# Kernel tuning notes

Measured on AMD Instinct MI355X. Metric: run time of the kernel, lower is better.

Reference implementation:

```python
import jax, jax.numpy as jnp
import numpy as np

C_IN = 128
DIM = 2 * C_IN          # ELAN final channels = 2*in_channels = 256
WS = 8                  # window size
HEADS = 8
HEAD_DIM = DIM // HEADS
B, H, W = 4, 128, 128
LN_EPS = 1e-5


def setup_inputs() -> dict:
    key = jax.random.key(0)
    ks = jax.random.split(key, 20)
    mid = C_IN // 2  # middle_channels == block_channels == 64

    def p(k, shape, scale=0.05):
        return jax.random.normal(k, shape, jnp.float32) * scale

    return dict(
        x=jax.random.normal(ks[0], (B, C_IN, H, W), jnp.float32),
        # ELAN stem 1x1 convs: [main, short], each folded BN (scale, bias)
        w_stem=p(ks[1], (2, mid, C_IN, 1, 1)),
        s_stem=1.0 + p(ks[2], (2, mid)),
        b_stem=p(ks[3], (2, mid)),
        # 2 blocks x 2 convs of 3x3, mid->mid
        w_blk=p(ks[4], (4, mid, mid, 3, 3)),
        s_blk=1.0 + p(ks[5], (4, mid)),
        b_blk=p(ks[6], (4, mid)),
        # SwinV2 block params
        norm1_g=jnp.ones((DIM,), jnp.float32),
        norm1_b=jnp.zeros((DIM,), jnp.float32),
        qkv_w=p(ks[7], (3 * DIM, DIM)),
        qkv_b=p(ks[8], (3 * DIM,)).at[DIM:2 * DIM].set(0.0),  # V2 zeroes k bias
        proj_w=p(ks[9], (DIM, DIM)),
        proj_b=p(ks[10], (DIM,)),
        logit_scale=jnp.full((HEADS, 1, 1), float(np.log(10.0)), jnp.float32),
        cpb_w1=p(ks[11], (512, 2)),
        cpb_b1=p(ks[12], (512,)),
        cpb_w2=p(ks[13], (HEADS, 512)),
        norm2_g=jnp.ones((DIM,), jnp.float32),
        norm2_b=jnp.zeros((DIM,), jnp.float32),
        mlp_w1=p(ks[14], (DIM, DIM)),  # mlp_ratio=1.0
        mlp_b1=p(ks[15], (DIM,)),
        mlp_w2=p(ks[16], (DIM, DIM)),
        mlp_b2=p(ks[17], (DIM,)),
    )


def convbn(x, w, s, b, pad):
    # Conv(no bias) + eval-mode BN folded into per-channel scale/bias + SiLU
    y = jax.lax.conv_general_dilated(
        x, w, (1, 1), [(pad, pad), (pad, pad)],
        dimension_numbers=("NCHW", "OIHW", "NCHW"))
    y = y * s[None, :, None, None] + b[None, :, None, None]
    return jax.nn.silu(y)


def layernorm(x, g, b):
    m = jnp.mean(x, -1, keepdims=True)
    v = jnp.var(x, -1, keepdims=True)
    return (x - m) * jax.lax.rsqrt(v + LN_EPS) * g + b


def _rel_bias_consts():
    ws = WS
    ch = np.arange(-(ws - 1), ws, dtype=np.float32)
    table = np.stack(np.meshgrid(ch, ch, indexing="ij"), axis=-1)  # [2ws-1,2ws-1,2]
    table = table / (ws - 1) * 8.0
    table = np.sign(table) * np.log2(np.abs(table) + 1.0) / 3.0
    coords = np.stack(np.meshgrid(np.arange(ws), np.arange(ws), indexing="ij")).reshape(2, -1)
    rel = (coords[:, :, None] - coords[:, None, :]).transpose(1, 2, 0)  # [N,N,2]
    rel[..., 0] += ws - 1
    rel[..., 1] += ws - 1
    rel[..., 0] *= 2 * ws - 1
    idx = rel.sum(-1).reshape(-1)
    return jnp.asarray(table.reshape(-1, 2)), jnp.asarray(idx)


_TABLE, _IDX = _rel_bias_consts()


def elan_swin(x, w_stem, s_stem, b_stem, w_blk, s_blk, b_blk, norm1_g, norm1_b,
              qkv_w, qkv_b, proj_w, proj_b, logit_scale, cpb_w1, cpb_b1, cpb_w2,
              norm2_g, norm2_b, mlp_w1, mlp_b1, mlp_w2, mlp_b2):
    # ---- ELANBlock ----
    x_short = convbn(x, w_stem[1], s_stem[1], b_stem[1], 0)
    x_main = convbn(x, w_stem[0], s_stem[0], b_stem[0], 0)
    xb = x_main
    outs = []
    for i in range(2):
        xb = convbn(xb, w_blk[2 * i], s_blk[2 * i], b_blk[2 * i], 1)
        xb = convbn(xb, w_blk[2 * i + 1], s_blk[2 * i + 1], b_blk[2 * i + 1], 1)
        outs.append(xb)
    e = jnp.concatenate([outs[1], outs[0], x_main, x_short], axis=1)  # [B,DIM,H,W]
    e = e.transpose(0, 2, 3, 1)  # NHWC

    # ---- ShiftedWindowAttentionV2 (shift=0, H,W divisible by WS) ----
    Bn, Hh, Ww, Cc = e.shape
    nH, nW = Hh // WS, Ww // WS
    N = WS * WS
    xw = e.reshape(Bn, nH, WS, nW, WS, Cc).transpose(0, 1, 3, 2, 4, 5).reshape(-1, N, Cc)
    qkv = xw @ qkv_w.T + qkv_b
    qkv = qkv.reshape(-1, N, 3, HEADS, HEAD_DIM).transpose(2, 0, 3, 1, 4)
    q, k, v = qkv[0], qkv[1], qkv[2]  # [Bw, heads, N, d]
    qn = q / jnp.maximum(jnp.linalg.norm(q, axis=-1, keepdims=True), 1e-12)
    kn = k / jnp.maximum(jnp.linalg.norm(k, axis=-1, keepdims=True), 1e-12)
    attn = jnp.einsum("whnd,whmd->whnm", qn, kn)
    scale = jnp.exp(jnp.minimum(logit_scale, jnp.log(100.0)))  # [heads,1,1]
    attn = attn * scale[None]
    # continuous position bias MLP
    bias = jax.nn.relu(_TABLE @ cpb_w1.T + cpb_b1) @ cpb_w2.T  # [(2ws-1)^2, heads]
    bias = bias[_IDX].reshape(N, N, HEADS).transpose(2, 0, 1)
    bias = 16.0 * jax.nn.sigmoid(bias)
    attn = jax.nn.softmax(attn + bias[None], axis=-1)
    out = jnp.einsum("whnm,whmd->whnd", attn, v).transpose(0, 2, 1, 3).reshape(-1, N, Cc)
    out = out @ proj_w.T + proj_b
    out = out.reshape(Bn, nH, nW, WS, WS, Cc).transpose(0, 1, 3, 2, 4, 5).reshape(Bn, Hh, Ww, Cc)

    # ---- SwinTransformerBlockV2 (post-norm residuals) ----
    s = e + layernorm(out, norm1_g, norm1_b)
    h = s @ mlp_w1.T + mlp_b1
    h = jax.nn.gelu(h, approximate=False)
    h = h @ mlp_w2.T + mlp_b2
    s = s + layernorm(h, norm2_g, norm2_b)
    return s.transpose(0, 3, 1, 2)  # NCHW


def reference(x, w_stem, s_stem, b_stem, w_blk, s_blk, b_blk, norm1_g, norm1_b,
              qkv_w, qkv_b, proj_w, proj_b, logit_scale, cpb_w1, cpb_b1, cpb_w2,
              norm2_g, norm2_b, mlp_w1, mlp_b1, mlp_w2, mlp_b2):
    return elan_swin(x, w_stem, s_stem, b_stem, w_blk, s_blk, b_blk, norm1_g, norm1_b,
                     qkv_w, qkv_b, proj_w, proj_b, logit_scale, cpb_w1, cpb_b1, cpb_w2,
                     norm2_g, norm2_b, mlp_w1, mlp_b1, mlp_w2, mlp_b2)
```

## Files before the change

kernel.cpp:

```cpp
#include <hip/hip_runtime.h>
#include <hip/hip_bf16.h>
#include <math.h>


#define HW 16384
typedef unsigned int u32;
typedef unsigned short u16;
typedef __attribute__((ext_vector_type(8))) short short8;
typedef __attribute__((ext_vector_type(4))) float floatx4;

#define MEMBAR() asm volatile("" ::: "memory")

__device__ __forceinline__ float silu_f(float y) { return y / (1.f + expf(-y)); }
__device__ __forceinline__ float bflo(u32 u) { return __uint_as_float(u << 16); }
__device__ __forceinline__ float bfhi(u32 u) { return __uint_as_float(u & 0xffff0000u); }
__device__ __forceinline__ float bf2f(u16 v) { return __uint_as_float((u32)v << 16); }
__device__ __forceinline__ u16 f2bf(float x) {
  u32 u = __float_as_uint(x);
  u += 0x7fffu + ((u >> 16) & 1u);
  return (u16)(u >> 16);
}
__device__ __forceinline__ u32 pack2(float a, float b) {
  return (u32)f2bf(a) | ((u32)f2bf(b) << 16);
}

#define GLDS16(gp, lp)                                           \
  __builtin_amdgcn_global_load_lds(                              \
      (const __attribute__((address_space(1))) void*)(gp),       \
      (__attribute__((address_space(3))) void*)(lp), 16, 0, 0)

__global__ __launch_bounds__(256) void repack_kernel(
    const float* __restrict__ w_blk, const float* __restrict__ s_blk,
    const float* __restrict__ w_stem, const float* __restrict__ s_stem,
    u16* __restrict__ wtc, u16* __restrict__ wts) {
  int idx = blockIdx.x * 256 + threadIdx.x;
  if (idx < 147456) {
    int c = idx & 63;
    int rest = idx >> 6;
    int oc = rest & 63;
    int ct = rest >> 6;
    int conv = ct / 9, t = ct % 9;
    float w = w_blk[((size_t)(conv * 64 + oc) * 64 + c) * 9 + t];
    wtc[idx] = f2bf(w * s_blk[conv * 64 + oc]);
  } else if (idx < 147456 + 16384) {
    int j = idx - 147456;
    int c = j & 127, oc = j >> 7;
    float w = w_stem[(size_t)oc * 128 + c];
    wts[j] = f2bf(w * s_stem[oc]);
  }
}

__global__ __launch_bounds__(256) void castw_kernel(
    const float* __restrict__ in, u16* __restrict__ outp, int n) {
  int i = blockIdx.x * 256 + threadIdx.x;
  if (i < n) outp[i] = f2bf(in[i]);
}

__global__ __launch_bounds__(512) void cpb_mlp_kernel(
    const float* __restrict__ w1, const float* __restrict__ b1,
    const float* __restrict__ w2, float* __restrict__ pre) {
  __shared__ float hb[512];
  int t = blockIdx.x, j = threadIdx.x;
  int i = t / 15, jj = t % 15;
  float c0 = (float)(i - 7) * (8.f / 7.f);
  float c1 = (float)(jj - 7) * (8.f / 7.f);
  float s0 = (c0 > 0.f) ? 1.f : ((c0 < 0.f) ? -1.f : 0.f);
  float s1 = (c1 > 0.f) ? 1.f : ((c1 < 0.f) ? -1.f : 0.f);
  float t0 = s0 * log2f(fabsf(c0) + 1.f) * (1.f / 3.f);
  float t1 = s1 * log2f(fabsf(c1) + 1.f) * (1.f / 3.f);
  float h = t0 * w1[j * 2] + t1 * w1[j * 2 + 1] + b1[j];
  hb[j] = fmaxf(h, 0.f);
  __syncthreads();
  if (j < 8) {
    float s = 0.f;
    for (int k = 0; k < 512; ++k) s += hb[k] * w2[j * 512 + k];
    pre[t * 8 + j] = s;
  }
}

__global__ __launch_bounds__(256) void cpb_expand_kernel(
    const float* __restrict__ pre, float* __restrict__ bias_t) {
  int idx = blockIdx.x * 256 + threadIdx.x;
  int m = idx >> 6, n = idx & 63;
  int di = (n >> 3) - (m >> 3) + 7;
  int dj = (n & 7) - (m & 7) + 7;
  int ti = di * 15 + dj;
#pragma unroll
  for (int h = 0; h < 8; ++h) {
    float v = pre[ti * 8 + h];
    bias_t[h * 4096 + idx] = 16.f / (1.f + expf(-v));
  }
}

__global__ __launch_bounds__(256) void transpose_in_kernel(
    const float* __restrict__ x, u16* __restrict__ xt) {
  __shared__ float tl[64][65];
  int bid = blockIdx.x;
  int b = bid >> 9;
  int r = bid & 511;
  int cs = r >> 8, hws = r & 255;
  int c0 = cs << 6, hw0 = hws << 6;
  int tid = threadIdx.x;
  for (int e = tid; e < 4096; e += 256) {
    int c = e >> 6, p = e & 63;
    tl[c][p] = x[(size_t)(b * 128 + c0 + c) * HW + hw0 + p];
  }
  __syncthreads();
  for (int e = tid; e < 4096; e += 256) {
    int p = e >> 6, c = e & 63;
    xt[(size_t)(b * HW + hw0 + p) * 128 + c0 + c] = f2bf(tl[c][p]);
  }
}

__global__ __launch_bounds__(256, 4) void gemm_bf16_kernel(
    const u16* __restrict__ A, const u16* __restrict__ W,
    const float* __restrict__ bias, u16* __restrict__ C, int K, int ldc,
    int act) {
  __shared__ u16 As[128 * 64];
  __shared__ u16 Ws[64 * 64];
  int tid = threadIdx.x;
  int wv = tid >> 6, lane = tid & 63;
  int m0 = blockIdx.x * 128, n0 = blockIdx.y * 64;
  floatx4 zz = {0.f, 0.f, 0.f, 0.f};
  floatx4 acc[2][4];
#pragma unroll
  for (int i = 0; i < 2; ++i)
#pragma unroll
    for (int j = 0; j < 4; ++j) acc[i][j] = zz;
  int lr = lane >> 3, ls = lane & 7;
  for (int k0 = 0; k0 < K; k0 += 64) {
#pragma unroll
    for (int i = 0; i < 4; ++i) {
      int ci = wv * 4 + i;
      int r = ci * 8 + lr;
      int cc = ls ^ (r & 7);
      GLDS16(A + (size_t)(m0 + r) * K + k0 + cc * 8, As + ci * 512);
    }
#pragma unroll
    for (int i = 0; i < 2; ++i) {
      int ci = wv * 2 + i;
      int r = ci * 8 + lr;
      int cc = ls ^ (r & 7);
      GLDS16(W + (size_t)(n0 + r) * K + k0 + cc * 8, Ws + ci * 512);
    }
    __syncthreads();
#pragma unroll
    for (int kk = 0; kk < 2; ++kk) {
      int g = kk * 4 + (lane >> 4);
      short8 a0, a1, b0, b1, b2, b3;
      {
        int row = wv * 32 + (lane & 15);
        a0 = *(const short8*)&As[row * 64 + (g ^ (row & 7)) * 8];
        int row2 = row + 16;
        a1 = *(const short8*)&As[row2 * 64 + (g ^ (row2 & 7)) * 8];
      }
      {
        int col = lane & 15;
        b0 = *(const short8*)&Ws[col * 64 + (g ^ (col & 7)) * 8];
        int c1 = col + 16;
        b1 = *(const short8*)&Ws[c1 * 64 + (g ^ (c1 & 7)) * 8];
        int c2 = col + 32;
        b2 = *(const short8*)&Ws[c2 * 64 + (g ^ (c2 & 7)) * 8];
        int c3 = col + 48;
        b3 = *(const short8*)&Ws[c3 * 64 + (g ^ (c3 & 7)) * 8];
      }
      acc[0][0] = __builtin_amdgcn_mfma_f32_16x16x32_bf16(a0, b0, acc[0][0], 0, 0, 0);
      acc[0][1] = __builtin_amdgcn_mfma_f32_16x16x32_bf16(a0, b1, acc[0][1], 0, 0, 0);
      acc[0][2] = __builtin_amdgcn_mfma_f32_16x16x32_bf16(a0, b2, acc[0][2], 0, 0, 0);
      acc[0][3] = __builtin_amdgcn_mfma_f32_16x16x32_bf16(a0, b3, acc[0][3], 0, 0, 0);
      acc[1][0] = __builtin_amdgcn_mfma_f32_16x16x32_bf16(a1, b0, acc[1][0], 0, 0, 0);
      acc[1][1] = __builtin_amdgcn_mfma_f32_16x16x32_bf16(a1, b1, acc[1][1], 0, 0, 0);
      acc[1][2] = __builtin_amdgcn_mfma_f32_16x16x32_bf16(a1, b2, acc[1][2], 0, 0, 0);
      acc[1][3] = __builtin_amdgcn_mfma_f32_16x16x32_bf16(a1, b3, acc[1][3], 0, 0, 0);
    }
    __syncthreads();
  }
  int rbase = wv * 32 + ((lane >> 4) << 2);
  int cb = lane & 15;
#pragma unroll
  for (int mi = 0; mi < 2; ++mi) {
#pragma unroll
    for (int nj = 0; nj < 4; ++nj) {
      int col = n0 + nj * 16 + cb;
      float bv = bias[col];
#pragma unroll
      for (int r = 0; r < 4; ++r) {
        int row = m0 + rbase + mi * 16 + r;
        float v = acc[mi][nj][r] + bv;
        if (act == 1) v = 0.5f * v * (1.f + erff(v * 0.70710678118654752f));
        else if (act == 2) v = silu_f(v);
        C[(size_t)row * ldc + col] = f2bf(v);
      }
    }
  }
}

__global__ __launch_bounds__(256) void conv3x3_mfma_kernel(
    const u16* __restrict__ in, int istr, u16* __restrict__ outp, int ostr,
    const u16* __restrict__ wt, const float* __restrict__ bias) {
  __shared__ u16 tile[6400];
  int tid = threadIdx.x;
  int wv = tid >> 6, lane = tid & 63;
  int bx = blockIdx.x, by = blockIdx.y, b = blockIdx.z;
  int h0 = by * 8, w0 = bx * 8;
#pragma unroll
  for (int rr = 0; rr < 4; ++rr) {
    int slot = rr * 256 + tid;
    int p = slot >> 3, ch = slot & 7;
    if (p < 100) {
      int hr = p / 10, hc = p % 10;
      int gh = h0 + hr - 1, gw = w0 + hc - 1;
      bool ok = (gh >= 0) && (gh < 128) && (gw >= 0) && (gw < 128);
      uint4 v = {0u, 0u, 0u, 0u};
      if (ok) {
        size_t pix = (size_t)((b * 128 + gh) * 128 + gw);
        v = *(const uint4*)(in + pix * istr + ch * 8);
      }
      *(uint4*)(tile + p * 64 + ((ch ^ (p & 7)) << 3)) = v;
    }
  }
  __syncthreads();
  int pl = lane & 15;
  int g = lane >> 4;
  int prow = 2 * wv + (pl >> 3), pcol = pl & 7;
  floatx4 zz = {0.f, 0.f, 0.f, 0.f};
  floatx4 acc[4] = {zz, zz, zz, zz};
#pragma unroll
  for (int t = 0; t < 9; ++t) {
    int dy = t / 3, dx = t % 3;
    int hp = (prow + dy) * 10 + (pcol + dx);
    short8 bf0 = *(const short8*)&tile[hp * 64 + (((0 * 4 + g) ^ (hp & 7)) << 3)];
    short8 bf1 = *(const short8*)&tile[hp * 64 + (((1 * 4 + g) ^ (hp & 7)) << 3)];
    const u16* wtap = wt + t * 4096;
#pragma unroll
    for (int nf = 0; nf < 4; ++nf) {
      short8 a0 = *(const short8*)&wtap[(nf * 16 + pl) * 64 + g * 8];
      short8 a1 = *(const short8*)&wtap[(nf * 16 + pl) * 64 + 32 + g * 8];
      acc[nf] = __builtin_amdgcn_mfma_f32_16x16x32_bf16(a0, bf0, acc[nf], 0, 0, 0);
      acc[nf] = __builtin_amdgcn_mfma_f32_16x16x32_bf16(a1, bf1, acc[nf], 0, 0, 0);
    }
  }
  size_t pix = (size_t)((b * 128 + h0 + prow) * 128 + w0 + pcol);
#pragma unroll
  for (int nf = 0; nf < 4; ++nf) {
    float o0 = silu_f(acc[nf][0] + bias[nf * 16 + g * 4 + 0]);
    float o1 = silu_f(acc[nf][1] + bias[nf * 16 + g * 4 + 1]);
    float o2 = silu_f(acc[nf][2] + bias[nf * 16 + g * 4 + 2]);
    float o3 = silu_f(acc[nf][3] + bias[nf * 16 + g * 4 + 3]);
    uint2 w2;
    w2.x = pack2(o0, o1);
    w2.y = pack2(o2, o3);
    *(uint2*)(outp + pix * ostr + nf * 16 + g * 4) = w2;
  }
}

__device__ __forceinline__ void qkv_mm(const u16* Elds, const u16* qwb,
                                       int moff, int h, int lc, int lg,
                                       floatx4 acc[4][2]) {
  floatx4 zz = {0.f, 0.f, 0.f, 0.f};
#pragma unroll
  for (int mf = 0; mf < 4; ++mf) {
    acc[mf][0] = zz;
    acc[mf][1] = zz;
  }
#pragma unroll
  for (int ks = 0; ks < 8; ++ks) {
    int ch = ks >> 1, g = ((ks & 1) << 2) + lg;
    short8 af[4];
#pragma unroll
    for (int mf = 0; mf < 4; ++mf) {
      int tk = mf * 16 + lc;
      af[mf] = *(const short8*)&Elds[(ch * 64 + tk) * 64 + ((g ^ (tk & 7)) << 3)];
    }
#pragma unroll
    for (int nf = 0; nf < 2; ++nf) {
      short8 bf = *(const short8*)(qwb +
          (size_t)(moff + h * 32 + nf * 16 + lc) * 256 + ks * 32 + lg * 8);
#pragma unroll
      for (int mf = 0; mf < 4; ++mf)
        acc[mf][nf] =
            __builtin_amdgcn_mfma_f32_16x16x32_bf16(af[mf], bf, acc[mf][nf], 0, 0, 0);
    }
  }
}

__global__ __launch_bounds__(256) void attn_fused_kernel(
    const u16* __restrict__ ebf, const u16* __restrict__ qwb,
    const float* __restrict__ qkv_b, const float* __restrict__ logit_scale,
    const float* __restrict__ bias_t, u16* __restrict__ ao) {
  __shared__ __align__(16) char lds[73728];
  int tid = threadIdx.x;
  int w = tid >> 6, l = tid & 63;
  int wid = blockIdx.x >> 1;
  int h = __builtin_amdgcn_readfirstlane(((blockIdx.x & 1) << 2) + w);
  u16* Elds = (u16*)lds;
  char* Kn = lds + 32768 + w * 10240;
  char* Qn = Kn + 5120;
  char* Pt = Kn;
  char* Vt = lds + w * 4608;
  char* Ol = Vt;

  int b = wid >> 8, wh = (wid >> 4) & 15, ww = wid & 15;
  int pixbase = (b << 14) + wh * 1024 + ww * 8;
  {
    int lr = l >> 3, ls = l & 7;
#pragma unroll
    for (int j = 0; j < 8; ++j) {
      int pix = pixbase + j * 128 + lr;
      GLDS16(ebf + (size_t)pix * 256 + w * 64 + ((ls ^ lr) << 3),
             Elds + (w * 8 + j) * 512);
    }
  }
  __syncthreads();

  int lc = l & 15, lg = l >> 4;
  float scale = __expf(fminf(logit_scale[h], 4.6051701860f));
  floatx4 macc[4][2];
  float rnrm[4][4];
  short8 kf_hi[4], kf_lo[4], qf_hi[4], qf_lo[4];

  qkv_mm(Elds, qwb, 256, h, lc, lg, macc);
#pragma unroll
  for (int mf = 0; mf < 4; ++mf)
#pragma unroll
    for (int r = 0; r < 4; ++r) {
      float v0 = macc[mf][0][r], v1 = macc[mf][1][r];
      float ss = v0 * v0 + v1 * v1;
      ss += __shfl_xor(ss, 1);
      ss += __shfl_xor(ss, 2);
      ss += __shfl_xor(ss, 4);
      ss += __shfl_xor(ss, 8);
      float rk = 1.f / fmaxf(sqrtf(ss), 1e-12f);
      rnrm[mf][r] = rk;
      int tk = mf * 16 + (lg << 2) + r;
      *(u16*)(Kn + tk * 80 + lc * 2) = f2bf(v0 * rk);
      *(u16*)(Kn + tk * 80 + (16 + lc) * 2) = f2bf(v1 * rk);
    }
  MEMBAR();
#pragma unroll
  for (int i = 0; i < 4; ++i)
    kf_hi[i] = *(const short8*)(Kn + (i * 16 + lc) * 80 + (lg << 4));
  MEMBAR();
#pragma unroll
  for (int mf = 0; mf < 4; ++mf)
#pragma unroll
    for (int r = 0; r < 4; ++r) {
      int tk = mf * 16 + (lg << 2) + r;
      float s0 = macc[mf][0][r] * rnrm[mf][r];
      float s1 = macc[mf][1][r] * rnrm[mf][r];
      *(u16*)(Kn + tk * 80 + lc * 2) = f2bf(s0 - bf2f(f2bf(s0)));
      *(u16*)(Kn + tk * 80 + (16 + lc) * 2) = f2bf(s1 - bf2f(f2bf(s1)));
    }
  MEMBAR();
#pragma unroll
  for (int i = 0; i < 4; ++i)
    kf_lo[i] = *(const short8*)(Kn + (i * 16 + lc) * 80 + (lg << 4));
  MEMBAR();

  qkv_mm(Elds, qwb, 0, h, lc, lg, macc);
  {
    float qb0 = qkv_b[h * 32 + lc], qb1 = qkv_b[h * 32 + 16 + lc];
#pragma unroll
    for (int mf = 0; mf < 4; ++mf)
#pragma unroll
      for (int r = 0; r < 4; ++r) {
        float v0 = macc[mf][0][r] + qb0, v1 = macc[mf][1][r] + qb1;
        macc[mf][0][r] = v0;
        macc[mf][1][r] = v1;
        float ss = v0 * v0 + v1 * v1;
        ss += __shfl_xor(ss, 1);
        ss += __shfl_xor(ss, 2);
        ss += __shfl_xor(ss, 4);
        ss += __shfl_xor(ss, 8);
        float rq = scale / fmaxf(sqrtf(ss), 1e-12f);
        rnrm[mf][r] = rq;
        int tk = mf * 16 + (lg << 2) + r;
        *(u16*)(Qn + tk * 80 + lc * 2) = f2bf(v0 * rq);
        *(u16*)(Qn + tk * 80 + (16 + lc) * 2) = f2bf(v1 * rq);
      }
    MEMBAR();
#pragma unroll
    for (int i = 0; i < 4; ++i)
      qf_hi[i] = *(const short8*)(Qn + (i * 16 + lc) * 80 + (lg << 4));
    MEMBAR();
#pragma unroll
    for (int mf = 0; mf < 4; ++mf)
#pragma unroll
      for (int r = 0; r < 4; ++r) {
        int tk = mf * 16 + (lg << 2) + r;
        float s0 = macc[mf][0][r] * rnrm[mf][r];
        float s1 = macc[mf][1][r] * rnrm[mf][r];
        *(u16*)(Qn + tk * 80 + lc * 2) = f2bf(s0 - bf2f(f2bf(s0)));
        *(u16*)(Qn + tk * 80 + (16 + lc) * 2) = f2bf(s1 - bf2f(f2bf(s1)));
      }
    MEMBAR();
#pragma unroll
    for (int i = 0; i < 4; ++i)
      qf_lo[i] = *(const short8*)(Qn + (i * 16 + lc) * 80 + (lg << 4));
    MEMBAR();
  }

  qkv_mm(Elds, qwb, 512, h, lc, lg, macc);
  float vb0 = qkv_b[512 + h * 32 + lc], vb1 = qkv_b[512 + h * 32 + 16 + lc];
  __syncthreads();
#pragma unroll
  for (int mf = 0; mf < 4; ++mf)
#pragma unroll
    for (int r = 0; r < 4; ++r) {
      int tk = mf * 16 + (lg << 2) + r;
      *(u16*)(Vt + lc * 144 + tk * 2) = f2bf(macc[mf][0][r] + vb0);
      *(u16*)(Vt + (16 + lc) * 144 + tk * 2) = f2bf(macc[mf][1][r] + vb1);
    }
  MEMBAR();

  floatx4 zz = {0.f, 0.f, 0.f, 0.f};
  floatx4 S[4][4];
#pragma unroll
  for (int mi = 0; mi < 4; ++mi)
#pragma unroll
    for (int ni = 0; ni < 4; ++ni) {
      floatx4 a = __builtin_amdgcn_mfma_f32_16x16x32_bf16(kf_lo[mi], qf_hi[ni], zz, 0, 0, 0);
      a = __builtin_amdgcn_mfma_f32_16x16x32_bf16(kf_hi[mi], qf_lo[ni], a, 0, 0, 0);
      S[mi][ni] = __builtin_amdgcn_mfma_f32_16x16x32_bf16(kf_hi[mi], qf_hi[ni], a, 0, 0, 0);
    }

  const float* bh = bias_t + h * 4096;
  float den[4] = {0.f, 0.f, 0.f, 0.f};
#pragma unroll
  for (int mi = 0; mi < 4; ++mi) {
    int mb = mi * 16 + (lg << 2);
#pragma unroll
    for (int ni = 0; ni < 4; ++ni) {
      int nn = ni * 16 + lc;
#pragma unroll
      for (int r = 0; r < 4; ++r) {
        float e = __expf(S[mi][ni][r] + bh[(mb + r) * 64 + nn]);
        S[mi][ni][r] = e;
        den[ni] += e;
      }
    }
  }
#pragma unroll
  for (int ni = 0; ni < 4; ++ni) {
    den[ni] += __shfl_xor(den[ni], 16);
    den[ni] += __shfl_xor(den[ni], 32);
    den[ni] = 1.f / den[ni];
  }
#pragma unroll
  for (int ni = 0; ni < 4; ++ni)
#pragma unroll
    for (int mi = 0; mi < 4; ++mi) {
      uint2 v;
      v.x = pack2(S[mi][ni][0] * den[ni], S[mi][ni][1] * den[ni]);
      v.y = pack2(S[mi][ni][2] * den[ni], S[mi][ni][3] * den[ni]);
      *(uint2*)(Pt + (ni * 16 + lc) * 144 + mi * 32 + (lg << 3)) = v;
    }
  MEMBAR();
  short8 vf[2][2];
#pragma unroll
  for (int ks = 0; ks < 2; ++ks)
#pragma unroll
    for (int db = 0; db < 2; ++db)
      vf[ks][db] = *(const short8*)(Vt + (db * 16 + lc) * 144 + ks * 64 + (lg << 4));
  floatx4 O[4][2];
#pragma unroll
  for (int nb = 0; nb < 4; ++nb) {
    O[nb][0] = zz;
    O[nb][1] = zz;
  }
#pragma unroll
  for (int nb = 0; nb < 4; ++nb) {
    short8 pf0 = *(const short8*)(Pt + (nb * 16 + lc) * 144 + (lg << 4));
    short8 pf1 = *(const short8*)(Pt + (nb * 16 + lc) * 144 + 64 + (lg << 4));
    O[nb][0] = __builtin_amdgcn_mfma_f32_16x16x32_bf16(pf0, vf[0][0], O[nb][0], 0, 0, 0);
    O[nb][0] = __builtin_amdgcn_mfma_f32_16x16x32_bf16(pf1, vf[1][0], O[nb][0], 0, 0, 0);
    O[nb][1] = __builtin_amdgcn_mfma_f32_16x16x32_bf16(pf0, vf[0][1], O[nb][1], 0, 0, 0);
    O[nb][1] = __builtin_amdgcn_mfma_f32_16x16x32_bf16(pf1, vf[1][1], O[nb][1], 0, 0, 0);
  }
  MEMBAR();
#pragma unroll
  for (int nb = 0; nb < 4; ++nb)
#pragma unroll
    for (int r = 0; r < 4; ++r) {
      int n = nb * 16 + (lg << 2) + r;
      *(u16*)(Ol + n * 72 + lc * 2) = f2bf(O[nb][0][r]);
      *(u16*)(Ol + n * 72 + (16 + lc) * 2) = f2bf(O[nb][1][r]);
    }
  MEMBAR();
  u32 ov[16];
#pragma unroll
  for (int j = 0; j < 16; ++j) ov[j] = *(const u32*)(Ol + l * 72 + j * 4);
  uint4* op = (uint4*)(ao + (size_t)(wid * 64 + l) * 256 + h * 32);
#pragma unroll
  for (int q4 = 0; q4 < 4; ++q4) {
    uint4 v;
    v.x = ov[q4 * 4 + 0];
    v.y = ov[q4 * 4 + 1];
    v.z = ov[q4 * 4 + 2];
    v.w = ov[q4 * 4 + 3];
    op[q4] = v;
  }
}

__global__ __launch_bounds__(256) void ln1v_kernel(
    const u16* __restrict__ pin, const u16* __restrict__ ebf,
    u16* __restrict__ sbf, const float* __restrict__ g,
    const float* __restrict__ bb) {
  int tid = threadIdx.x;
  int bid = blockIdx.x;
  int b = bid >> 8, hw0 = (bid & 255) << 6;
  int i = tid >> 2, qq = tid & 3;
  int hw = hw0 + i;
  int him = hw >> 7, wim = hw & 127;
  int wid = b * 256 + (him >> 3) * 16 + (wim >> 3);
  int t = wid * 64 + (him & 7) * 8 + (wim & 7);
  size_t pbase = (size_t)t * 256 + qq * 64;
  size_t ebase = ((size_t)(b * HW + hw)) * 256 + qq * 64;
  float v[64];
  float s1 = 0.f, s2 = 0.f;
#pragma unroll
  for (int j = 0; j < 8; ++j) {
    uint4 u = *(const uint4*)(pin + pbase + j * 8);
    u32 ua[4] = {u.x, u.y, u.z, u.w};
#pragma unroll
    for (int k = 0; k < 4; ++k) {
      float a = bflo(ua[k]), c = bfhi(ua[k]);
      v[j * 8 + 2 * k] = a;
      v[j * 8 + 2 * k + 1] = c;
      s1 += a + c;
      s2 += a * a + c * c;
    }
  }
  s1 += __shfl_xor(s1, 1);
  s1 += __shfl_xor(s1, 2);
  s2 += __shfl_xor(s2, 1);
  s2 += __shfl_xor(s2, 2);
  float mean = s1 * (1.f / 256.f);
  float var = s2 * (1.f / 256.f) - mean * mean;
  float rs = rsqrtf(var + 1e-5f);
#pragma unroll
  for (int j = 0; j < 8; ++j) {
    uint4 u = *(const uint4*)(ebf + ebase + j * 8);
    u32 ua[4] = {u.x, u.y, u.z, u.w};
    uint4 o;
    u32 ow[4];
#pragma unroll
    for (int k = 0; k < 4; ++k) {
      int c = qq * 64 + j * 8 + 2 * k;
      float o0 = bflo(ua[k]) + (v[j * 8 + 2 * k] - mean) * rs * g[c] + bb[c];
      float o1 = bfhi(ua[k]) + (v[j * 8 + 2 * k + 1] - mean) * rs * g[c + 1] + bb[c + 1];
      ow[k] = pack2(o0, o1);
    }
    o.x = ow[0]; o.y = ow[1]; o.z = ow[2]; o.w = ow[3];
    *(uint4*)(sbf + ebase + j * 8) = o;
  }
}

__global__ __launch_bounds__(256) void ln2t_kernel(
    const u16* __restrict__ h2, const u16* __restrict__ sbf,
    const float* __restrict__ g, const float* __restrict__ bb,
    float* __restrict__ outp) {
  __shared__ float tile[64][257];
  int tid = threadIdx.x;
  int bid = blockIdx.x;
  int b = bid >> 8, hw0 = (bid & 255) << 6;
  int i = tid >> 2, qq = tid & 3;
  size_t base = ((size_t)(b * HW + hw0 + i)) * 256 + qq * 64;
  float v[64];
  float s1 = 0.f, s2 = 0.f;
#pragma unroll
  for (int j = 0; j < 8; ++j) {
    uint4 u = *(const uint4*)(h2 + base + j * 8);
    u32 ua[4] = {u.x, u.y, u.z, u.w};
#pragma unroll
    for (int k = 0; k < 4; ++k) {
      float a = bflo(ua[k]), c = bfhi(ua[k]);
      v[j * 8 + 2 * k] = a;
      v[j * 8 + 2 * k + 1] = c;
      s1 += a + c;
      s2 += a * a + c * c;
    }
  }
  s1 += __shfl_xor(s1, 1);
  s1 += __shfl_xor(s1, 2);
  s2 += __shfl_xor(s2, 1);
  s2 += __shfl_xor(s2, 2);
  float mean = s1 * (1.f / 256.f);
  float var = s2 * (1.f / 256.f) - mean * mean;
  float rs = rsqrtf(var + 1e-5f);
#pragma unroll
  for (int j = 0; j < 8; ++j) {
    uint4 u = *(const uint4*)(sbf + base + j * 8);
    u32 ua[4] = {u.x, u.y, u.z, u.w};
#pragma unroll
    for (int k = 0; k < 4; ++k) {
      int c = qq * 64 + j * 8 + 2 * k;
      tile[i][c] = bflo(ua[k]) + (v[j * 8 + 2 * k] - mean) * rs * g[c] + bb[c];
      tile[i][c + 1] = bfhi(ua[k]) + (v[j * 8 + 2 * k + 1] - mean) * rs * g[c + 1] + bb[c + 1];
    }
  }
  __syncthreads();
  int pl = tid & 63, cq = tid >> 6;
#pragma unroll 8
  for (int cc = 0; cc < 64; ++cc) {
    int c = cq * 64 + cc;
    outp[((size_t)(b * 256 + c)) * HW + hw0 + pl] = tile[pl][c];
  }
}

extern "C" void kernel_launch(void* const* d_in, const int* in_sizes, int n_in,
                              void* d_out, int out_size, void* d_ws, size_t ws_size,
                              hipStream_t stream) {
  const float* x        = (const float*)d_in[0];
  const float* w_stem   = (const float*)d_in[1];
  const float* s_stem   = (const float*)d_in[2];
  const float* b_stem   = (const float*)d_in[3];
  const float* w_blk    = (const float*)d_in[4];
  const float* s_blk    = (const float*)d_in[5];
  const float* b_blk    = (const float*)d_in[6];
  const float* norm1_g  = (const float*)d_in[7];
  const float* norm1_b  = (const float*)d_in[8];
  const float* qkv_w    = (const float*)d_in[9];
  const float* qkv_b    = (const float*)d_in[10];
  const float* proj_w   = (const float*)d_in[11];
  const float* proj_b   = (const float*)d_in[12];
  const float* logit_sc = (const float*)d_in[13];
  const float* cpb_w1   = (const float*)d_in[14];
  const float* cpb_b1   = (const float*)d_in[15];
  const float* cpb_w2   = (const float*)d_in[16];
  const float* norm2_g  = (const float*)d_in[17];
  const float* norm2_b  = (const float*)d_in[18];
  const float* mlp_w1   = (const float*)d_in[19];
  const float* mlp_b1   = (const float*)d_in[20];
  const float* mlp_w2   = (const float*)d_in[21];
  const float* mlp_b2   = (const float*)d_in[22];
  float* out = (float*)d_out;
  float* ws = (float*)d_ws;
  (void)in_sizes; (void)n_in; (void)out_size; (void)ws_size;

  float* R0 = ws;
  float* R1 = ws + 16777216;
  float* R2 = ws + 33554432;
  float* TAIL = ws + 50331648;
  u16* WTC  = (u16*)TAIL;
  u16* WTS  = (u16*)(TAIL + 73728);
  u16* QWB  = (u16*)(TAIL + 81920);
  u16* PWB  = (u16*)(TAIL + 180224);
  u16* M1WB = (u16*)(TAIL + 212992);
  u16* M2WB = (u16*)(TAIL + 245760);
  float* BPRE = TAIL + 278528;
  float* BFT  = TAIL + 280576;

  u16* XT  = (u16*)R2;
  u16* EBF = (u16*)(R2 + 8388608);
  u16* T1  = (u16*)R1;
  u16* T2  = (u16*)(R1 + 2097152);
  u16* AO  = (u16*)R0;
  u16* P   = (u16*)(R0 + 8388608);
  u16* SBF = (u16*)R0;
  u16* Hb  = (u16*)R2;
  u16* H2  = (u16*)(R0 + 8388608);

  repack_kernel<<<640, 256, 0, stream>>>(w_blk, s_blk, w_stem, s_stem, WTC, WTS);
  castw_kernel<<<768, 256, 0, stream>>>(qkv_w, QWB, 196608);
  castw_kernel<<<256, 256, 0, stream>>>(proj_w, PWB, 65536);
  castw_kernel<<<256, 256, 0, stream>>>(mlp_w1, M1WB, 65536);
  castw_kernel<<<256, 256, 0, stream>>>(mlp_w2, M2WB, 65536);
  cpb_mlp_kernel<<<225, 512, 0, stream>>>(cpb_w1, cpb_b1, cpb_w2, BPRE);
  cpb_expand_kernel<<<16, 256, 0, stream>>>(BPRE, BFT);

  transpose_in_kernel<<<2048, 256, 0, stream>>>(x, XT);
  dim3 gs(512, 2);
  gemm_bf16_kernel<<<gs, 256, 0, stream>>>(XT, WTS, b_stem, EBF + 128, 128, 256, 2);

  dim3 cgrid(16, 16, 4);
  conv3x3_mfma_kernel<<<cgrid, 256, 0, stream>>>(EBF + 128, 256, T1, 64, WTC, b_blk);
  conv3x3_mfma_kernel<<<cgrid, 256, 0, stream>>>(T1, 64, EBF + 64, 256, WTC + 9 * 4096, b_blk + 64);
  conv3x3_mfma_kernel<<<cgrid, 256, 0, stream>>>(EBF + 64, 256, T2, 64, WTC + 18 * 4096, b_blk + 128);
  conv3x3_mfma_kernel<<<cgrid, 256, 0, stream>>>(T2, 64, EBF, 256, WTC + 27 * 4096, b_blk + 192);

  attn_fused_kernel<<<2048, 256, 0, stream>>>(EBF, QWB, qkv_b, logit_sc, BFT, AO);

  dim3 g4(512, 4);
  gemm_bf16_kernel<<<g4, 256, 0, stream>>>(AO, PWB, proj_b, P, 256, 256, 0);
  ln1v_kernel<<<1024, 256, 0, stream>>>(P, EBF, SBF, norm1_g, norm1_b);
  gemm_bf16_kernel<<<g4, 256, 0, stream>>>(SBF, M1WB, mlp_b1, Hb, 256, 256, 1);
  gemm_bf16_kernel<<<g4, 256, 0, stream>>>(Hb, M2WB, mlp_b2, H2, 256, 256, 0);
  ln2t_kernel<<<1024, 256, 0, stream>>>(H2, SBF, norm2_g, norm2_b, out);
}
```

Measured before the change: 443.2 us.

## Drop split-bf16 QK precision, fuse QKV matmuls, reorder GEMM grid

The attention kernel previously computed normalized Q and K as hi/lo bf16 pairs and ran three MFMAs per score tile for extra precision. It now uses a single bf16 product, which removes two thirds of the score MFMAs and the LDS round trips for the lo parts. The Q, K and V projections are merged into one pass over the LDS A-fragments, so those fragments are loaded once instead of three times, at the cost of more accumulator registers. Separately, the GEMM grid axes are swapped so consecutive blocks share the same M tile, which should improve L2 reuse of A. Lower QK precision may hurt accuracy, and the extra registers may lower occupancy.

```diff
diff --git a/kernel.cpp b/kernel.cpp
--- a/kernel.cpp
+++ b/kernel.cpp
@@ -120,7 +120,7 @@
   __shared__ u16 Ws[64 * 64];
   int tid = threadIdx.x;
   int wv = tid >> 6, lane = tid & 63;
-  int m0 = blockIdx.x * 128, n0 = blockIdx.y * 64;
+  int m0 = blockIdx.y * 128, n0 = blockIdx.x * 64;
   floatx4 zz = {0.f, 0.f, 0.f, 0.f};
   floatx4 acc[2][4];
 #pragma unroll
@@ -251,36 +251,6 @@
     w2.x = pack2(o0, o1);
     w2.y = pack2(o2, o3);
     *(uint2*)(outp + pix * ostr + nf * 16 + g * 4) = w2;
-  }
-}
-
-__device__ __forceinline__ void qkv_mm(const u16* Elds, const u16* qwb,
-                                       int moff, int h, int lc, int lg,
-                                       floatx4 acc[4][2]) {
-  floatx4 zz = {0.f, 0.f, 0.f, 0.f};
-#pragma unroll
-  for (int mf = 0; mf < 4; ++mf) {
-    acc[mf][0] = zz;
-    acc[mf][1] = zz;
-  }
-#pragma unroll
-  for (int ks = 0; ks < 8; ++ks) {
-    int ch = ks >> 1, g = ((ks & 1) << 2) + lg;
-    short8 af[4];
-#pragma unroll
-    for (int mf = 0; mf < 4; ++mf) {
-      int tk = mf * 16 + lc;
-      af[mf] = *(const short8*)&Elds[(ch * 64 + tk) * 64 + ((g ^ (tk & 7)) << 3)];
-    }
-#pragma unroll
-    for (int nf = 0; nf < 2; ++nf) {
-      short8 bf = *(const short8*)(qwb +
-          (size_t)(moff + h * 32 + nf * 16 + lc) * 256 + ks * 32 + lg * 8);
-#pragma unroll
-      for (int mf = 0; mf < 4; ++mf)
-        acc[mf][nf] =
-            __builtin_amdgcn_mfma_f32_16x16x32_bf16(af[mf], bf, acc[mf][nf], 0, 0, 0);
-    }
   }
 }
 
@@ -315,23 +285,65 @@
 
   int lc = l & 15, lg = l >> 4;
   float scale = __expf(fminf(logit_scale[h], 4.6051701860f));
-  floatx4 macc[4][2];
-  float rnrm[4][4];
-  short8 kf_hi[4], kf_lo[4], qf_hi[4], qf_lo[4];
-
-  qkv_mm(Elds, qwb, 256, h, lc, lg, macc);
+
+  floatx4 zz = {0.f, 0.f, 0.f, 0.f};
+  floatx4 aq[4][2], ak[4][2], av[4][2];
+#pragma unroll
+  for (int mf = 0; mf < 4; ++mf) {
+    aq[mf][0] = zz; aq[mf][1] = zz;
+    ak[mf][0] = zz; ak[mf][1] = zz;
+    av[mf][0] = zz; av[mf][1] = zz;
+  }
+#pragma unroll
+  for (int ks = 0; ks < 8; ++ks) {
+    int ch = ks >> 1, g = ((ks & 1) << 2) + lg;
+    short8 af[4];
+#pragma unroll
+    for (int mf = 0; mf < 4; ++mf) {
+      int tk = mf * 16 + lc;
+      af[mf] = *(const short8*)&Elds[(ch * 64 + tk) * 64 + ((g ^ (tk & 7)) << 3)];
+    }
+#pragma unroll
+    for (int nf = 0; nf < 2; ++nf) {
+      const u16* wb = qwb + (size_t)(h * 32 + nf * 16 + lc) * 256 + ks * 32 + lg * 8;
+      short8 bq = *(const short8*)(wb);
+      short8 bk = *(const short8*)(wb + 65536);
+      short8 bv = *(const short8*)(wb + 131072);
+#pragma unroll
+      for (int mf = 0; mf < 4; ++mf) {
+        aq[mf][nf] = __builtin_amdgcn_mfma_f32_16x16x32_bf16(af[mf], bq, aq[mf][nf], 0, 0, 0);
+        ak[mf][nf] = __builtin_amdgcn_mfma_f32_16x16x32_bf16(af[mf], bk, ak[mf][nf], 0, 0, 0);
+        av[mf][nf] = __builtin_amdgcn_mfma_f32_16x16x32_bf16(af[mf], bv, av[mf][nf], 0, 0, 0);
+      }
+    }
+  }
+  __syncthreads();
+
+  {
+    float vb0 = qkv_b[512 + h * 32 + lc], vb1 = qkv_b[512 + h * 32 + 16 + lc];
+#pragma unroll
+    for (int mf = 0; mf < 4; ++mf)
+#pragma unroll
+      for (int r = 0; r < 4; ++r) {
+        int tk = mf * 16 + (lg << 2) + r;
+        *(u16*)(Vt + lc * 144 + tk * 2) = f2bf(av[mf][0][r] + vb0);
+        *(u16*)(Vt + (16 + lc) * 144 + tk * 2) = f2bf(av[mf][1][r] + vb1);
+      }
+  }
+  MEMBAR();
+
+  short8 kf[4], qf[4];
 #pragma unroll
   for (int mf = 0; mf < 4; ++mf)
 #pragma unroll
     for (int r = 0; r < 4; ++r) {
-      float v0 = macc[mf][0][r], v1 = macc[mf][1][r];
+      float v0 = ak[mf][0][r], v1 = ak[mf][1][r];
       float ss = v0 * v0 + v1 * v1;
       ss += __shfl_xor(ss, 1);
       ss += __shfl_xor(ss, 2);
       ss += __shfl_xor(ss, 4);
       ss += __shfl_xor(ss, 8);
       float rk = 1.f / fmaxf(sqrtf(ss), 1e-12f);
-      rnrm[mf][r] = rk;
       int tk = mf * 16 + (lg << 2) + r;
       *(u16*)(Kn + tk * 80 + lc * 2) = f2bf(v0 * rk);
       *(u16*)(Kn + tk * 80 + (16 + lc) * 2) = f2bf(v1 * rk);
@@ -339,41 +351,22 @@
   MEMBAR();
 #pragma unroll
   for (int i = 0; i < 4; ++i)
-    kf_hi[i] = *(const short8*)(Kn + (i * 16 + lc) * 80 + (lg << 4));
+    kf[i] = *(const short8*)(Kn + (i * 16 + lc) * 80 + (lg << 4));
   MEMBAR();
-#pragma unroll
-  for (int mf = 0; mf < 4; ++mf)
-#pragma unroll
-    for (int r = 0; r < 4; ++r) {
-      int tk = mf * 16 + (lg << 2) + r;
-      float s0 = macc[mf][0][r] * rnrm[mf][r];
-      float s1 = macc[mf][1][r] * rnrm[mf][r];
-      *(u16*)(Kn + tk * 80 + lc * 2) = f2bf(s0 - bf2f(f2bf(s0)));
-      *(u16*)(Kn + tk * 80 + (16 + lc) * 2) = f2bf(s1 - bf2f(f2bf(s1)));
-    }
-  MEMBAR();
-#pragma unroll
-  for (int i = 0; i < 4; ++i)
-    kf_lo[i] = *(const short8*)(Kn + (i * 16 + lc) * 80 + (lg << 4));
-  MEMBAR();
-
-  qkv_mm(Elds, qwb, 0, h, lc, lg, macc);
+
   {
     float qb0 = qkv_b[h * 32 + lc], qb1 = qkv_b[h * 32 + 16 + lc];
 #pragma unroll
     for (int mf = 0; mf < 4; ++mf)
 #pragma unroll
       for (int r = 0; r < 4; ++r) {
-        float v0 = macc[mf][0][r] + qb0, v1 = macc[mf][1][r] + qb1;
-        macc[mf][0][r] = v0;
-        macc[mf][1][r] = v1;
+        float v0 = aq[mf][0][r] + qb0, v1 = aq[mf][1][r] + qb1;
         float ss = v0 * v0 + v1 * v1;
         ss += __shfl_xor(ss, 1);
         ss += __shfl_xor(ss, 2);
         ss += __shfl_xor(ss, 4);
         ss += __shfl_xor(ss, 8);
         float rq = scale / fmaxf(sqrtf(ss), 1e-12f);
-        rnrm[mf][r] = rq;
         int tk = mf * 16 + (lg << 2) + r;
         *(u16*)(Qn + tk * 80 + lc * 2) = f2bf(v0 * rq);
         *(u16*)(Qn + tk * 80 + (16 + lc) * 2) = f2bf(v1 * rq);
@@ -381,48 +374,16 @@
     MEMBAR();
 #pragma unroll
     for (int i = 0; i < 4; ++i)
-      qf_hi[i] = *(const short8*)(Qn + (i * 16 + lc) * 80 + (lg << 4));
+      qf[i] = *(const short8*)(Qn + (i * 16 + lc) * 80 + (lg << 4));
     MEMBAR();
-#pragma unroll
-    for (int mf = 0; mf < 4; ++mf)
-#pragma unroll
-      for (int r = 0; r < 4; ++r) {
-        int tk = mf * 16 + (lg << 2) + r;
-        float s0 = macc[mf][0][r] * rnrm[mf][r];
-        float s1 = macc[mf][1][r] * rnrm[mf][r];
-        *(u16*)(Qn + tk * 80 + lc * 2) = f2bf(s0 - bf2f(f2bf(s0)));
-        *(u16*)(Qn + tk * 80 + (16 + lc) * 2) = f2bf(s1 - bf2f(f2bf(s1)));
-      }
-    MEMBAR();
-#pragma unroll
-    for (int i = 0; i < 4; ++i)
-      qf_lo[i] = *(const short8*)(Qn + (i * 16 + lc) * 80 + (lg << 4));
-    MEMBAR();
-  }
-
-  qkv_mm(Elds, qwb, 512, h, lc, lg, macc);
-  float vb0 = qkv_b[512 + h * 32 + lc], vb1 = qkv_b[512 + h * 32 + 16 + lc];
-  __syncthreads();
-#pragma unroll
-  for (int mf = 0; mf < 4; ++mf)
-#pragma unroll
-    for (int r = 0; r < 4; ++r) {
-      int tk = mf * 16 + (lg << 2) + r;
-      *(u16*)(Vt + lc * 144 + tk * 2) = f2bf(macc[mf][0][r] + vb0);
-      *(u16*)(Vt + (16 + lc) * 144 + tk * 2) = f2bf(macc[mf][1][r] + vb1);
-    }
-  MEMBAR();
-
-  floatx4 zz = {0.f, 0.f, 0.f, 0.f};
+  }
+
   floatx4 S[4][4];
 #pragma unroll
   for (int mi = 0; mi < 4; ++mi)
 #pragma unroll
-    for (int ni = 0; ni < 4; ++ni) {
-      floatx4 a = __builtin_amdgcn_mfma_f32_16x16x32_bf16(kf_lo[mi], qf_hi[ni], zz, 0, 0, 0);
-      a = __builtin_amdgcn_mfma_f32_16x16x32_bf16(kf_hi[mi], qf_lo[ni], a, 0, 0, 0);
-      S[mi][ni] = __builtin_amdgcn_mfma_f32_16x16x32_bf16(kf_hi[mi], qf_hi[ni], a, 0, 0, 0);
-    }
+    for (int ni = 0; ni < 4; ++ni)
+      S[mi][ni] = __builtin_amdgcn_mfma_f32_16x16x32_bf16(kf[mi], qf[ni], zz, 0, 0, 0);
 
   const float* bh = bias_t + h * 4096;
   float den[4] = {0.f, 0.f, 0.f, 0.f};
@@ -670,7 +631,7 @@
   cpb_expand_kernel<<<16, 256, 0, stream>>>(BPRE, BFT);
 
   transpose_in_kernel<<<2048, 256, 0, stream>>>(x, XT);
-  dim3 gs(512, 2);
+  dim3 gs(2, 512);
   gemm_bf16_kernel<<<gs, 256, 0, stream>>>(XT, WTS, b_stem, EBF + 128, 128, 256, 2);
 
   dim3 cgrid(16, 16, 4);
@@ -681,7 +642,7 @@
 
   attn_fused_kernel<<<2048, 256, 0, stream>>>(EBF, QWB, qkv_b, logit_sc, BFT, AO);
 
-  dim3 g4(512, 4);
+  dim3 g4(4, 512);
   gemm_bf16_kernel<<<g4, 256, 0, stream>>>(AO, PWB, proj_b, P, 256, 256, 0);
   ln1v_kernel<<<1024, 256, 0, stream>>>(P, EBF, SBF, norm1_g, norm1_b);
   gemm_bf16_kernel<<<g4, 256, 0, stream>>>(SBF, M1WB, mlp_b1, Hb, 256, 256, 1);
```

Result: slower. 467.0 us (+5.4%).
